# Performance work log

Measured on AMD Instinct MI355X. Metric: run time of the kernel, lower is better.

The kernel has to match this reference:

```python
import jax, jax.numpy as jnp
import numpy as np

B, S = 256, 512
E, K, D, H = 20000, 500, 128, 128  # num_exercises, num_skills, embed_dim, hidden_dim


def setup_inputs() -> dict:
    key = jax.random.key(0)
    ks = jax.random.split(key, 24)
    def lin(k, fan_in, fan_out):
        k1, k2 = jax.random.split(k)
        lim = 1.0 / np.sqrt(fan_in)
        W = jax.random.uniform(k1, (fan_in, fan_out), jnp.float32, -lim, lim)
        b = jax.random.uniform(k2, (fan_out,), jnp.float32, -lim, lim)
        return W, b
    def xavier(k, n, d):
        lim = np.sqrt(6.0 / (n + d))
        return jax.random.uniform(k, (n, d), jnp.float32, -lim, lim)
    W_time, b_time = lin(ks[0], 1, D)
    W_int, b_int = lin(ks[1], 4 * D, D)
    W_b1, b_b1 = lin(ks[2], 2, H)
    W_b2, b_b2 = lin(ks[3], H, H)
    W_learn, b_learn = lin(ks[4], H + D + 1 + H + H, H)
    W_forget, b_forget = lin(ks[5], H + D + H + H, H)
    W_pred, b_pred = lin(ks[6], H + D, 1)
    return {
        "exercise_seq": jax.random.randint(ks[7], (B, S), 0, E),
        "skill_seq": jax.random.randint(ks[8], (B, S), 0, K),
        "response_seq": jax.random.randint(ks[9], (B, S), 0, 2),
        "time_seq": jax.random.uniform(ks[10], (B, S), jnp.float32),
        "interval_seq": jax.random.uniform(ks[11], (B, S), jnp.float32),
        "attempt_seq": jax.random.uniform(ks[12], (B, S), jnp.float32),
        "hint_seq": jax.random.uniform(ks[13], (B, S), jnp.float32),
        "q_matrix": jax.random.uniform(ks[14], (E, K), jnp.float32),
        "exercise_emb": xavier(ks[15], E, D),
        "skill_emb": xavier(ks[16], K, D),
        "response_emb": xavier(ks[17], 2, D),
        "W_time": W_time, "b_time": b_time,
        "W_int": W_int, "b_int": b_int,
        "W_b1": W_b1, "b_b1": b_b1,
        "W_b2": W_b2, "b_b2": b_b2,
        "W_learn": W_learn, "b_learn": b_learn,
        "W_forget": W_forget, "b_forget": b_forget,
        "W_pred": W_pred, "b_pred": b_pred,
    }


def _forward(exercise_seq, skill_seq, response_seq, time_seq, interval_seq,
             attempt_seq, hint_seq, q_matrix,
             exercise_emb, skill_emb, response_emb,
             W_time, b_time, W_int, b_int, W_b1, b_b1, W_b2, b_b2,
             W_learn, b_learn, W_forget, b_forget, W_pred, b_pred):
    e = exercise_emb[exercise_seq]            # [B,S,D]
    s = skill_emb[skill_seq]                  # [B,S,D]
    r = response_emb[response_seq]            # [B,S,D]
    t = time_seq[..., None] * W_time[0] + b_time  # Linear(1,D): [B,S,D]
    inter = jax.nn.relu(jnp.concatenate([e, s, t, r], axis=-1) @ W_int + b_int)  # [B,S,D]
    beh_in = jnp.stack([attempt_seq, hint_seq], axis=-1)  # [B,S,2]
    beh = jax.nn.relu(beh_in @ W_b1 + b_b1) @ W_b2 + b_b2  # [B,S,H]
    # fifth gate input segment is behavior[:, t] except zeros at the last step
    beh2 = beh.at[:, -1, :].set(0.0)

    # time-major for scan
    xs = (jnp.swapaxes(e, 0, 1), jnp.swapaxes(inter, 0, 1),
          jnp.swapaxes(beh, 0, 1), jnp.swapaxes(beh2, 0, 1),
          jnp.swapaxes(interval_seq, 0, 1))
    h0 = jnp.zeros((e.shape[0], H), e.dtype)

    def step(h, x):
        ce, ci, cb, nb, iv = x
        lg = jax.nn.sigmoid(
            jnp.concatenate([h, ci, iv[:, None], cb, nb], axis=-1) @ W_learn + b_learn)
        fg = jax.nn.sigmoid(
            jnp.concatenate([h, ci, lg, cb], axis=-1) @ W_forget + b_forget)
        h = lg + fg * h
        p = jax.nn.sigmoid(jnp.concatenate([h, ce], axis=-1) @ W_pred + b_pred)
        return h, p[:, 0]

    _, preds = jax.lax.scan(step, h0, xs)  # [S,B]
    return jnp.swapaxes(preds, 0, 1)       # [B,S]


def reference(exercise_seq, skill_seq, response_seq, time_seq, interval_seq,
              attempt_seq, hint_seq, q_matrix,
              exercise_emb, skill_emb, response_emb,
              W_time, b_time, W_int, b_int, W_b1, b_b1, W_b2, b_b2,
              W_learn, b_learn, W_forget, b_forget, W_pred, b_pred):
    return _forward(exercise_seq, skill_seq, response_seq, time_seq, interval_seq,
                    attempt_seq, hint_seq, q_matrix,
                    exercise_emb, skill_emb, response_emb,
                    W_time, b_time, W_int, b_int, W_b1, b_b1, W_b2, b_b2,
                    W_learn, b_learn, W_forget, b_forget, W_pred, b_pred)
```

## Files before the change

### kernel.cpp

```cpp
#include <hip/hip_runtime.h>
#include <hip/hip_fp16.h>

#define BB 256
#define SS 512
#define EE_N 20000
#define NEGLAM -1.442695041f
typedef _Float16 f16;
typedef __attribute__((ext_vector_type(8))) _Float16 half8;
typedef __attribute__((ext_vector_type(4))) _Float16 half4_;
typedef __attribute__((ext_vector_type(2))) _Float16 half2_;
typedef __attribute__((ext_vector_type(4))) float f32x4;

__device__ __forceinline__ float sigm(float x) {
  return __builtin_amdgcn_rcpf(1.0f + __builtin_amdgcn_exp2f(NEGLAM * x));
}
__device__ __forceinline__ float sigm_pre(float s) {
  return __builtin_amdgcn_rcpf(1.0f + __builtin_amdgcn_exp2f(s));
}

__global__ __launch_bounds__(256) void k012_prep(
    const float* ex_emb, const float* skill_emb, const float* response_emb,
    const float* W_time, const float* b_time,
    const float* W_int, const float* b_int,
    const float* W_b2, const float* b_b2,
    const float* W_learn, const float* b_learn,
    const float* W_forget, const float* b_forget,
    const float* W_pred,
    float* Ee, float* Se, float* Re, float* Te, float* cbias,
    float* c_lg, float* c_fg, float* fix_l,
    float* M_lnb, f16* Wfrag, float* pe, f16* Bfrag) {
  __shared__ float es[8 * 128];
  int blk = blockIdx.x, tid = threadIdx.x;
  if (blk < 2500) {
    *(float4*)&es[tid * 4] = *(const float4*)&ex_emb[(size_t)blk * 1024 + tid * 4];
    __syncthreads();
    int d = tid & 127, rg = tid >> 7;
    float a0 = 0, a1 = 0, a2 = 0, a3 = 0;
    for (int k = 0; k < 128; k++) {
      float w = W_int[k * 128 + d];
      a0 += es[(rg * 4 + 0) * 128 + k] * w;
      a1 += es[(rg * 4 + 1) * 128 + k] * w;
      a2 += es[(rg * 4 + 2) * 128 + k] * w;
      a3 += es[(rg * 4 + 3) * 128 + k] * w;
    }
    Ee[((size_t)blk * 8 + rg * 4 + 0) * 128 + d] = a0;
    Ee[((size_t)blk * 8 + rg * 4 + 1) * 128 + d] = a1;
    Ee[((size_t)blk * 8 + rg * 4 + 2) * 128 + d] = a2;
    Ee[((size_t)blk * 8 + rg * 4 + 3) * 128 + d] = a3;
  } else if (blk < 3388) {
    int b0 = blk - 2500, j = tid;
    if (j < 128) {
      if (b0 < 500) {
        float a = 0.f;
        for (int k = 0; k < 128; k++) a += skill_emb[b0 * 128 + k] * W_int[(128 + k) * 128 + j];
        Se[b0 * 128 + j] = a;
      } else if (b0 < 502) {
        int i = b0 - 500; float a = 0.f;
        for (int k = 0; k < 128; k++) a += response_emb[i * 128 + k] * W_int[(384 + k) * 128 + j];
        Re[i * 128 + j] = a;
      } else if (b0 == 502) {
        float a = 0.f, c = 0.f;
        for (int k = 0; k < 128; k++) {
          float w = W_int[(256 + k) * 128 + j];
          a += W_time[k] * w; c += b_time[k] * w;
        }
        Te[j] = a; cbias[j] = b_int[j] + c;
      } else if (b0 < 503 + 128) {
        int k = b0 - 503;
        int kt = k >> 5, gg = (k >> 3) & 3, e = k & 7;
        int nct = j >> 4, cc = j & 15;
        float vL = NEGLAM * W_learn[(128 + k) * 128 + j];
        float vF = NEGLAM * W_forget[(128 + k) * 128 + j];
        Bfrag[((size_t)((nct * 8 + kt) * 64) + gg * 16 + cc) * 8 + e] = (f16)vL;
        Bfrag[((size_t)(((8 + nct) * 8 + kt) * 64) + gg * 16 + cc) * 8 + e] = (f16)vF;
      } else if (b0 < 631 + 128) {
        int k2 = b0 - 631; float a = 0.f, c = 0.f;
        for (int m = 0; m < 128; m++) {
          float w = W_b2[k2 * 128 + m];
          a += w * (W_learn[(257 + m) * 128 + j] + W_learn[(385 + m) * 128 + j]);
          c += w * W_forget[(384 + m) * 128 + j];
        }
        int krow = 128 + k2;
        int kt = krow >> 5, gg = (krow >> 3) & 3, e = krow & 7;
        int nct = j >> 4, cc = j & 15;
        Bfrag[((size_t)((nct * 8 + kt) * 64) + gg * 16 + cc) * 8 + e] = (f16)(NEGLAM * a);
        Bfrag[((size_t)(((8 + nct) * 8 + kt) * 64) + gg * 16 + cc) * 8 + e] = (f16)(NEGLAM * c);
      } else if (b0 < 759 + 128) {
        int k = b0 - 759; float a = 0.f;
        for (int m = 0; m < 128; m++) a += W_b2[k * 128 + m] * W_learn[(385 + m) * 128 + j];
        M_lnb[k * 128 + j] = NEGLAM * a;
      } else {
        float a = 0.f, c = 0.f, f = 0.f;
        for (int m = 0; m < 128; m++) {
          float w = b_b2[m];
          a += w * (W_learn[(257 + m) * 128 + j] + W_learn[(385 + m) * 128 + j]);
          c += w * W_forget[(384 + m) * 128 + j];
          f += w * W_learn[(385 + m) * 128 + j];
        }
        c_lg[j] = NEGLAM * (b_learn[j] + a);
        c_fg[j] = NEGLAM * (b_forget[j] + c);
        fix_l[j] = NEGLAM * f;
      }
    }
  } else if (blk < 3484) {
    int b2 = blk - 3388;
    if (tid < 64) {
      int mat = b2 >> 5, rem = b2 & 31, w = rem >> 2, t4 = rem & 3;
      int lane = tid, cc = lane & 15, gg = lane >> 4;
      const float* src = (mat == 0) ? W_learn : (mat == 1 ? W_forget : W_forget + 256 * 128);
      f16* dst = Wfrag + ((size_t)b2 * 64 + lane) * 8;
      #pragma unroll
      for (int e = 0; e < 8; e++) {
        int k = t4 * 32 + gg * 8 + e;
        int j = 16 * w + cc;
        dst[e] = (f16)(NEGLAM * src[k * 128 + j]);
      }
    }
  } else {
    int b3 = blk - 3484;
    int w = tid >> 6, l = tid & 63, g = l >> 4, li = l & 15;
    int row = b3 * 16 + w * 4 + g;
    const float4* ep = (const float4*)(ex_emb + (size_t)row * 128 + li * 8);
    const float4* wp = (const float4*)(W_pred + 128 + li * 8);
    float4 e0 = ep[0], e1 = ep[1], w0 = wp[0], w1 = wp[1];
    float s = e0.x * w0.x + e0.y * w0.y + e0.z * w0.z + e0.w * w0.w
            + e1.x * w1.x + e1.y * w1.y + e1.z * w1.z + e1.w * w1.w;
    #pragma unroll
    for (int m = 1; m < 16; m <<= 1) s += __shfl_xor(s, m);
    if (li == 0) pe[row] = s;
  }
}

__global__ __launch_bounds__(512) void k3_gemm_mfma(
    const int* ex_seq, const int* sk_seq, const int* re_seq,
    const float* time_seq, const float* interval_seq,
    const float* att_seq, const float* hint_seq,
    const float* W_b1, const float* b_b1,
    const float* Wiv,
    const float* Ee, const float* Se, const float* Re,
    const float* Te, const float* cbias,
    const float* c_lg, const float* c_fg,
    const f16* Bfrag, f16* PRE) {
  __shared__ _Float16 Ah[64 * 256];
  __shared__ float ivs[64];
  int tid = threadIdx.x;
  int w = tid >> 6, lane = tid & 63;
  int c = lane & 15, g = lane >> 4;
  int rowbase = blockIdx.x * 64;

  half8 bfr[2][8];
  const half8* bp = (const half8*)Bfrag;
  #pragma unroll
  for (int ncl = 0; ncl < 2; ncl++)
    #pragma unroll
    for (int kt = 0; kt < 8; kt++)
      bfr[ncl][kt] = bp[((size_t)((w * 2 + ncl) * 8 + kt)) * 64 + lane];

  {
    int r = tid & 63, seg = tid >> 6;
    int row = rowbase + r;
    if (seg == 0) ivs[r] = interval_seq[row];
    char* ab = (char*)Ah;
    if (seg < 4) {
      int ex = ex_seq[row], sk = sk_seq[row], rp = re_seq[row];
      float tm = time_seq[row];
      const float4* ee = (const float4*)(Ee + (size_t)ex * 128 + seg * 32);
      const float4* se = (const float4*)(Se + (size_t)sk * 128 + seg * 32);
      const float4* re = (const float4*)(Re + (size_t)rp * 128 + seg * 32);
      const float4* te = (const float4*)(Te + seg * 32);
      const float4* cb = (const float4*)(cbias + seg * 32);
      #pragma unroll
      for (int i8 = 0; i8 < 4; i8++) {
        half8 hv;
        #pragma unroll
        for (int q = 0; q < 2; q++) {
          float4 e4 = ee[i8 * 2 + q], s4 = se[i8 * 2 + q], r4 = re[i8 * 2 + q];
          float4 t4 = te[i8 * 2 + q], c4 = cb[i8 * 2 + q];
          hv[q * 4 + 0] = (_Float16)fmaxf(e4.x + s4.x + tm * t4.x + r4.x + c4.x, 0.f);
          hv[q * 4 + 1] = (_Float16)fmaxf(e4.y + s4.y + tm * t4.y + r4.y + c4.y, 0.f);
          hv[q * 4 + 2] = (_Float16)fmaxf(e4.z + s4.z + tm * t4.z + r4.z + c4.z, 0.f);
          hv[q * 4 + 3] = (_Float16)fmaxf(e4.w + s4.w + tm * t4.w + r4.w + c4.w, 0.f);
        }
        int k0 = seg * 32 + i8 * 8;
        int byte = r * 512 + k0 * 2; byte ^= ((r & 7) << 4);
        *(half8*)(ab + byte) = hv;
      }
    } else {
      int k2b_ = (seg - 4) * 32;
      float at = att_seq[row], hi = hint_seq[row];
      const float4* wa = (const float4*)(W_b1 + k2b_);
      const float4* wh = (const float4*)(W_b1 + 128 + k2b_);
      const float4* bb = (const float4*)(b_b1 + k2b_);
      #pragma unroll
      for (int i8 = 0; i8 < 4; i8++) {
        half8 hv;
        #pragma unroll
        for (int q = 0; q < 2; q++) {
          float4 a4 = wa[i8 * 2 + q], h4 = wh[i8 * 2 + q], b4 = bb[i8 * 2 + q];
          hv[q * 4 + 0] = (_Float16)fmaxf(at * a4.x + hi * h4.x + b4.x, 0.f);
          hv[q * 4 + 1] = (_Float16)fmaxf(at * a4.y + hi * h4.y + b4.y, 0.f);
          hv[q * 4 + 2] = (_Float16)fmaxf(at * a4.z + hi * h4.z + b4.z, 0.f);
          hv[q * 4 + 3] = (_Float16)fmaxf(at * a4.w + hi * h4.w + b4.w, 0.f);
        }
        int k0 = 128 + k2b_ + i8 * 8;
        int byte = r * 512 + k0 * 2; byte ^= ((r & 7) << 4);
        *(half8*)(ab + byte) = hv;
      }
    }
  }
  __syncthreads();

  f32x4 acc[4][2] = {};
  const char* ab = (const char*)Ah;
  #pragma unroll
  for (int kt = 0; kt < 8; kt++) {
    #pragma unroll
    for (int mr = 0; mr < 4; mr++) {
      int byte = (mr * 16 + c) * 512 + kt * 64 + g * 16; byte ^= ((c & 7) << 4);
      half8 a = *(const half8*)(ab + byte);
      acc[mr][0] = __builtin_amdgcn_mfma_f32_16x16x32_f16(a, bfr[0][kt], acc[mr][0], 0, 0, 0);
      acc[mr][1] = __builtin_amdgcn_mfma_f32_16x16x32_f16(a, bfr[1][kt], acc[mr][1], 0, 0, 0);
    }
  }

  bool isL = (w < 4);
  float addc[2], wiv[2];
  int coff[2];
  #pragma unroll
  for (int ncl = 0; ncl < 2; ncl++) {
    int j = w * 32 + ncl * 16 + c;
    if (isL) { addc[ncl] = c_lg[j]; wiv[ncl] = NEGLAM * Wiv[j]; coff[ncl] = j * 4; }
    else     { addc[ncl] = c_fg[j - 128]; wiv[ncl] = 0.f; coff[ncl] = (j - 128) * 4 + 1; }
  }
  #pragma unroll
  for (int mr = 0; mr < 4; mr++) {
    #pragma unroll
    for (int rr = 0; rr < 4; rr++) {
      int rl = mr * 16 + g * 4 + rr;
      int row = rowbase + rl;
      float iv = ivs[rl];
      size_t base = (size_t)(row >> 9) * 131072 + (size_t)((row & 511) >> 1) * 512 + (row & 1) * 2;
      #pragma unroll
      for (int ncl = 0; ncl < 2; ncl++) {
        float v = acc[mr][ncl][rr] + addc[ncl] + iv * wiv[ncl];
        PRE[base + coff[ncl]] = (f16)v;
      }
    }
  }
}

__global__ __launch_bounds__(128) void k4_fix(
    const float* att_seq, const float* hint_seq,
    const float* W_b1, const float* b_b1,
    const float* M_lnb, const float* fix_l, f16* PRE) {
  int b = blockIdx.x, j = threadIdx.x;
  int row = b * SS + (SS - 1);
  __shared__ float rb_s[128];
  float v = att_seq[row] * W_b1[j] + hint_seq[row] * W_b1[128 + j] + b_b1[j];
  rb_s[j] = fmaxf(v, 0.f);
  __syncthreads();
  float a = fix_l[j];
  for (int m = 0; m < 128; m++) a += rb_s[m] * M_lnb[m * 128 + j];
  size_t idx = (size_t)b * 131072 + 255 * 512 + 2 + j * 4;
  PRE[idx] = (f16)((float)PRE[idx] - a);
}

#define BAR() asm volatile("s_waitcnt lgkmcnt(0)\n\ts_barrier" ::: "memory")
#define MF(A, B, C) __builtin_amdgcn_mfma_f32_16x16x32_f16(A, B, C, 0, 0, 0)

__global__ __launch_bounds__(512, 2) void k5_scan_mfma(
    const f16* __restrict__ PRE, const f16* __restrict__ Wfrag,
    f16* __restrict__ h_blk) {
  __shared__ _Float16 AhA[2048], AhB[2048], Alg[2048];
  int tid = threadIdx.x;
  int w = tid >> 6, lane = tid & 63;
  int c = lane & 15, g = lane >> 4;
  int b = blockIdx.x;

  if (tid < 256) {
    ((float4*)AhA)[tid] = make_float4(0.f, 0.f, 0.f, 0.f);
    ((float4*)AhB)[tid] = make_float4(0.f, 0.f, 0.f, 0.f);
    ((float4*)Alg)[tid] = make_float4(0.f, 0.f, 0.f, 0.f);
  }

  half8 bL[4], bFH[4], bFL[4];
  const half8* wp = (const half8*)Wfrag;
  #pragma unroll
  for (int t4 = 0; t4 < 4; t4++) {
    bL [t4] = wp[((0 * 8 + w) * 4 + t4) * 64 + lane];
    bFH[t4] = wp[((1 * 8 + w) * 4 + t4) * 64 + lane];
    bFL[t4] = wp[((2 * 8 + w) * 4 + t4) * 64 + lane];
  }

  int rd[4], wr[2];
  #pragma unroll
  for (int t4 = 0; t4 < 4; t4++) {
    int K8 = 4 * t4 + g;
    rd[t4] = K8 * 256 + (c ^ (K8 & 3)) * 16;
  }
  {
    int F = 16 * w + c;
    int K8w = F >> 3, q = K8w & 3;
    #pragma unroll
    for (int r = 0; r < 2; r++)
      wr[r] = K8w * 256 + ((4 * g + r) ^ q) * 16 + (F & 7) * 2;
  }

  int col = 16 * w + c;
  const f16* pr[2]; f16* hb4[2];
  float hstate[2] = {0.f, 0.f};
  float lgf[2];
  half4_ pA[4][2], pB[4][2];
  half4_ hb[2];
  #pragma unroll
  for (int r = 0; r < 2; r++) {
    int br = b * 8 + g * 2 + r;
    pr[r]  = PRE + (size_t)br * 131072 + col * 4;
    hb4[r] = h_blk + (size_t)br * 65536 + col * 4;
  }
  #pragma unroll
  for (int p = 0; p < 4; p++)
    #pragma unroll
    for (int r = 0; r < 2; r++)
      pA[p][r] = *(const half4_*)((const char*)pr[r] + p * 1024);
  __syncthreads();

  const f32x4 Z4 = {0.f, 0.f, 0.f, 0.f};

#define STEPX(SRC, DST, CB, P, PAR, LB, LOFF, I0, TIN, FLUSH, DOINC)             \
  {                                                                              \
    half8 ha[4];                                                                 \
    _Pragma("unroll")                                                            \
    for (int t4 = 0; t4 < 4; t4++)                                               \
      ha[t4] = *(const half8*)((const char*)(SRC) + rd[t4]);                     \
    if (DOINC) {                                                                 \
      _Pragma("unroll")                                                          \
      for (int r = 0; r < 2; r++) pr[r] += 4096;                                 \
    }                                                                            \
    { const int p_ = (I0) >> 1, r_ = (I0) & 1;                                   \
      LB[p_][r_] = *(const half4_*)((const char*)pr[r_] + (LOFF) + p_ * 1024); } \
    f32x4 cL = Z4, cF = Z4;                                                      \
    _Pragma("unroll")                                                            \
    for (int r = 0; r < 2; r++) {                                                \
      cL[r] = (float)CB[P][r][(PAR) * 2];                                        \
      cF[r] = (float)CB[P][r][(PAR) * 2 + 1];                                    \
    }                                                                            \
    __builtin_amdgcn_s_setprio(1);                                               \
    f32x4 aLa = cL, aLb = Z4;                                                    \
    aLa = MF(ha[0], bL[0], aLa);                                                 \
    aLb = MF(ha[2], bL[2], aLb);                                                 \
    aLa = MF(ha[1], bL[1], aLa);                                                 \
    aLb = MF(ha[3], bL[3], aLb);                                                 \
    __builtin_amdgcn_s_setprio(0);                                               \
    _Pragma("unroll")                                                            \
    for (int r = 0; r < 2; r++) {                                                \
      lgf[r] = sigm_pre(aLa[r] + aLb[r]);                                        \
      *(_Float16*)((char*)Alg + wr[r]) = (_Float16)lgf[r];                       \
    }                                                                            \
    BAR();                                                                       \
    half8 la[4];                                                                 \
    _Pragma("unroll")                                                            \
    for (int t4 = 0; t4 < 4; t4++)                                               \
      la[t4] = *(const half8*)((const char*)Alg + rd[t4]);                       \
    __builtin_amdgcn_s_setprio(1);                                               \
    f32x4 aHa = cF, aHb = Z4;                                                    \
    aHa = MF(ha[0], bFH[0], aHa);                                                \
    aHb = MF(ha[2], bFH[2], aHb);                                                \
    aHa = MF(ha[1], bFH[1], aHa);                                                \
    aHb = MF(ha[3], bFH[3], aHb);                                                \
    aHa = MF(la[0], bFL[0], aHa);                                                \
    aHb = MF(la[2], bFL[2], aHb);                                                \
    aHa = MF(la[1], bFL[1], aHa);                                                \
    aHb = MF(la[3], bFL[3], aHb);                                                \
    __builtin_amdgcn_s_setprio(0);                                               \
    _Pragma("unroll")                                                            \
    for (int r = 0; r < 2; r++) {                                                \
      float fg = sigm_pre(aHa[r] + aHb[r]);                                      \
      float hn = lgf[r] + fg * hstate[r];                                        \
      hstate[r] = hn;                                                            \
      _Float16 hv = (_Float16)hn;                                                \
      *(_Float16*)((char*)(DST) + wr[r]) = hv;                                   \
      hb[r][TIN] = hv;                                                           \
    }                                                                            \
    if ((FLUSH) >= 0) {                                                          \
      _Pragma("unroll")                                                          \
      for (int r = 0; r < 2; r++)                                                \
        *(half4_*)((char*)hb4[r] + (FLUSH)) = hb[r];                             \
    }                                                                            \
    BAR();                                                                       \
  }

  for (int it = 0; it < 32; ++it) {
    STEPX(AhA, AhB, pA, 0, 0, pB, 4096, 0, 0,   -1, 0);
    STEPX(AhB, AhA, pA, 0, 1, pB, 4096, 1, 1,   -1, 0);
    STEPX(AhA, AhB, pA, 1, 0, pB, 4096, 2, 2,   -1, 0);
    STEPX(AhB, AhA, pA, 1, 1, pB, 4096, 3, 3,    0, 0);
    STEPX(AhA, AhB, pA, 2, 0, pB, 4096, 4, 0,   -1, 0);
    STEPX(AhB, AhA, pA, 2, 1, pB, 4096, 5, 1,   -1, 0);
    STEPX(AhA, AhB, pA, 3, 0, pB, 4096, 6, 2,   -1, 0);
    STEPX(AhB, AhA, pA, 3, 1, pB, 4096, 7, 3, 1024, 0);
    STEPX(AhA, AhB, pB, 0, 0, pA, 0,    0, 0,   -1, 1);
    STEPX(AhB, AhA, pB, 0, 1, pA, 0,    1, 1,   -1, 0);
    STEPX(AhA, AhB, pB, 1, 0, pA, 0,    2, 2,   -1, 0);
    STEPX(AhB, AhA, pB, 1, 1, pA, 0,    3, 3, 2048, 0);
    STEPX(AhA, AhB, pB, 2, 0, pA, 0,    4, 0,   -1, 0);
    STEPX(AhB, AhA, pB, 2, 1, pA, 0,    5, 1,   -1, 0);
    STEPX(AhA, AhB, pB, 3, 0, pA, 0,    6, 2,   -1, 0);
    STEPX(AhB, AhA, pB, 3, 1, pA, 0,    7, 3, 3072, 0);
    #pragma unroll
    for (int r = 0; r < 2; r++) hb4[r] += 2048;
  }
#undef STEPX
}

__global__ __launch_bounds__(256) void k6_pred(
    const f16* h_blk, const int* ex_seq, const float* pe,
    const float* W_pred, const float* b_pred, float* out) {
  int tid = threadIdx.x;
  int wv = tid >> 6, lane = tid & 63;
  int task = blockIdx.x * 4 + wv;
  int br = task >> 7, t4b = task & 127;
  const f16* hp = h_blk + ((size_t)br * 128 + t4b) * 128 * 4;
  half4_ h0 = *(const half4_*)(hp + lane * 4);
  half4_ h1 = *(const half4_*)(hp + (lane + 64) * 4);
  float w0 = W_pred[lane], w1 = W_pred[lane + 64];
  float s[4];
  #pragma unroll
  for (int q = 0; q < 4; q++) s[q] = (float)h0[q] * w0 + (float)h1[q] * w1;
  #pragma unroll
  for (int m = 1; m < 64; m <<= 1) {
    #pragma unroll
    for (int q = 0; q < 4; q++) s[q] += __shfl_xor(s[q], m);
  }
  if (lane == 0) {
    int4 ex = *(const int4*)(ex_seq + (size_t)br * 512 + t4b * 4);
    float bb = b_pred[0];
    float4 o;
    o.x = sigm(s[0] + pe[ex.x] + bb);
    o.y = sigm(s[1] + pe[ex.y] + bb);
    o.z = sigm(s[2] + pe[ex.z] + bb);
    o.w = sigm(s[3] + pe[ex.w] + bb);
    *(float4*)(out + (size_t)br * 512 + t4b * 4) = o;
  }
}

extern "C" void kernel_launch(void* const* d_in, const int* in_sizes, int n_in,
                              void* d_out, int out_size, void* d_ws, size_t ws_size,
                              hipStream_t stream) {
  const int*   ex_seq   = (const int*)d_in[0];
  const int*   sk_seq   = (const int*)d_in[1];
  const int*   re_seq   = (const int*)d_in[2];
  const float* time_seq = (const float*)d_in[3];
  const float* interval_seq = (const float*)d_in[4];
  const float* att_seq  = (const float*)d_in[5];
  const float* hint_seq = (const float*)d_in[6];
  const float* ex_emb   = (const float*)d_in[8];
  const float* sk_emb   = (const float*)d_in[9];
  const float* re_emb   = (const float*)d_in[10];
  const float* W_time   = (const float*)d_in[11];
  const float* b_time   = (const float*)d_in[12];
  const float* W_int    = (const float*)d_in[13];
  const float* b_int    = (const float*)d_in[14];
  const float* W_b1     = (const float*)d_in[15];
  const float* b_b1     = (const float*)d_in[16];
  const float* W_b2     = (const float*)d_in[17];
  const float* b_b2     = (const float*)d_in[18];
  const float* W_learn  = (const float*)d_in[19];
  const float* b_learn  = (const float*)d_in[20];
  const float* W_forget = (const float*)d_in[21];
  const float* b_forget = (const float*)d_in[22];
  const float* W_pred   = (const float*)d_in[23];
  const float* b_pred   = (const float*)d_in[24];

  char* ws = (char*)d_ws;
  float* Ee    = (float*)(ws);
  float* Se    = (float*)(ws + 10240000);
  float* Re    = (float*)(ws + 10496000);
  float* Te    = (float*)(ws + 10497024);
  float* cbias = (float*)(ws + 10497536);
  float* c_lg  = (float*)(ws + 10498048);
  float* c_fg  = (float*)(ws + 10498560);
  float* fix_l = (float*)(ws + 10499072);
  float* M_lnb = (float*)(ws + 10761728);
  f16*   PRE   = (f16*)  (ws + 10827264);
  f16*   h_blk = (f16*)  (ws + 77936128);
  f16*   Wfrag = (f16*)  (ws + 111490560);
  float* pe    = (float*)(ws + 111588864);
  f16*   Bfrag = (f16*)  (ws + 77936128);

  k012_prep<<<dim3(4734), dim3(256), 0, stream>>>(
      ex_emb, sk_emb, re_emb, W_time, b_time, W_int, b_int, W_b2, b_b2,
      W_learn, b_learn, W_forget, b_forget, W_pred,
      Ee, Se, Re, Te, cbias, c_lg, c_fg, fix_l, M_lnb, Wfrag, pe, Bfrag);
  k3_gemm_mfma<<<dim3(2048), dim3(512), 0, stream>>>(
      ex_seq, sk_seq, re_seq, time_seq, interval_seq, att_seq, hint_seq,
      W_b1, b_b1, W_learn + 256 * 128, Ee, Se, Re, Te, cbias, c_lg, c_fg, Bfrag, PRE);
  k4_fix<<<dim3(256), dim3(128), 0, stream>>>(
      att_seq, hint_seq, W_b1, b_b1, M_lnb, fix_l, PRE);
  k5_scan_mfma<<<dim3(32), dim3(512), 0, stream>>>(PRE, Wfrag, h_blk);
  k6_pred<<<dim3(8192), dim3(256), 0, stream>>>(
      h_blk, ex_seq, pe, W_pred, b_pred, (float*)d_out);
}
```

Measured before the change: 328.3 us.

## Halve batch rows per scan block and double scan grid

The recurrent scan kernel now gives each block 4 batch rows instead of 8: each lane tracks one row rather than two, and the launch grid grows from 32 to 64 blocks. The serial per-step chain stays the same length, but more CUs run at once and each thread has less per-step epilogue work. In exchange, MFMA tiles are only a quarter populated (one valid row per 4-row group), and total weight fragment loads and LDS traffic double across blocks.

```diff
diff --git a/kernel.cpp b/kernel.cpp
--- a/kernel.cpp
+++ b/kernel.cpp
@@ -292,7 +292,7 @@
     bFL[t4] = wp[((2 * 8 + w) * 4 + t4) * 64 + lane];
   }
 
-  int rd[4], wr[2];
+  int rd[4], wr0;
   #pragma unroll
   for (int t4 = 0; t4 < 4; t4++) {
     int K8 = 4 * t4 + g;
@@ -301,28 +301,20 @@
   {
     int F = 16 * w + c;
     int K8w = F >> 3, q = K8w & 3;
-    #pragma unroll
-    for (int r = 0; r < 2; r++)
-      wr[r] = K8w * 256 + ((4 * g + r) ^ q) * 16 + (F & 7) * 2;
+    wr0 = K8w * 256 + ((4 * g) ^ q) * 16 + (F & 7) * 2;
   }
 
   int col = 16 * w + c;
-  const f16* pr[2]; f16* hb4[2];
-  float hstate[2] = {0.f, 0.f};
-  float lgf[2];
-  half4_ pA[4][2], pB[4][2];
-  half4_ hb[2];
-  #pragma unroll
-  for (int r = 0; r < 2; r++) {
-    int br = b * 8 + g * 2 + r;
-    pr[r]  = PRE + (size_t)br * 131072 + col * 4;
-    hb4[r] = h_blk + (size_t)br * 65536 + col * 4;
-  }
+  int br = b * 4 + g;
+  const f16* pr0 = PRE + (size_t)br * 131072 + col * 4;
+  f16* hb40 = h_blk + (size_t)br * 65536 + col * 4;
+  float hstate = 0.f;
+  float lgf0;
+  half4_ pA[4], pB[4];
+  half4_ hb0;
   #pragma unroll
   for (int p = 0; p < 4; p++)
-    #pragma unroll
-    for (int r = 0; r < 2; r++)
-      pA[p][r] = *(const half4_*)((const char*)pr[r] + p * 1024);
+    pA[p] = *(const half4_*)((const char*)pr0 + p * 1024);
   __syncthreads();
 
   const f32x4 Z4 = {0.f, 0.f, 0.f, 0.f};
@@ -333,18 +325,12 @@
     _Pragma("unroll")                                                            \
     for (int t4 = 0; t4 < 4; t4++)                                               \
       ha[t4] = *(const half8*)((const char*)(SRC) + rd[t4]);                     \
-    if (DOINC) {                                                                 \
-      _Pragma("unroll")                                                          \
-      for (int r = 0; r < 2; r++) pr[r] += 4096;                                 \
-    }                                                                            \
-    { const int p_ = (I0) >> 1, r_ = (I0) & 1;                                   \
-      LB[p_][r_] = *(const half4_*)((const char*)pr[r_] + (LOFF) + p_ * 1024); } \
+    if (DOINC) pr0 += 4096;                                                      \
+    if ((I0) >= 0)                                                               \
+      LB[(I0)] = *(const half4_*)((const char*)pr0 + (LOFF) + (I0) * 1024);      \
     f32x4 cL = Z4, cF = Z4;                                                      \
-    _Pragma("unroll")                                                            \
-    for (int r = 0; r < 2; r++) {                                                \
-      cL[r] = (float)CB[P][r][(PAR) * 2];                                        \
-      cF[r] = (float)CB[P][r][(PAR) * 2 + 1];                                    \
-    }                                                                            \
+    cL[0] = (float)CB[P][(PAR) * 2];                                             \
+    cF[0] = (float)CB[P][(PAR) * 2 + 1];                                         \
     __builtin_amdgcn_s_setprio(1);                                               \
     f32x4 aLa = cL, aLb = Z4;                                                    \
     aLa = MF(ha[0], bL[0], aLa);                                                 \
@@ -352,11 +338,8 @@
     aLa = MF(ha[1], bL[1], aLa);                                                 \
     aLb = MF(ha[3], bL[3], aLb);                                                 \
     __builtin_amdgcn_s_setprio(0);                                               \
-    _Pragma("unroll")                                                            \
-    for (int r = 0; r < 2; r++) {                                                \
-      lgf[r] = sigm_pre(aLa[r] + aLb[r]);                                        \
-      *(_Float16*)((char*)Alg + wr[r]) = (_Float16)lgf[r];                       \
-    }                                                                            \
+    lgf0 = sigm_pre(aLa[0] + aLb[0]);                                            \
+    *(_Float16*)((char*)Alg + wr0) = (_Float16)lgf0;                             \
     BAR();                                                                       \
     half8 la[4];                                                                 \
     _Pragma("unroll")                                                            \
@@ -373,42 +356,37 @@
     aHa = MF(la[1], bFL[1], aHa);                                                \
     aHb = MF(la[3], bFL[3], aHb);                                                \
     __builtin_amdgcn_s_setprio(0);                                               \
-    _Pragma("unroll")                                                            \
-    for (int r = 0; r < 2; r++) {                                                \
-      float fg = sigm_pre(aHa[r] + aHb[r]);                                      \
-      float hn = lgf[r] + fg * hstate[r];                                        \
-      hstate[r] = hn;                                                            \
+    {                                                                            \
+      float fg = sigm_pre(aHa[0] + aHb[0]);                                      \
+      float hn = lgf0 + fg * hstate;                                             \
+      hstate = hn;                                                               \
       _Float16 hv = (_Float16)hn;                                                \
-      *(_Float16*)((char*)(DST) + wr[r]) = hv;                                   \
-      hb[r][TIN] = hv;                                                           \
+      *(_Float16*)((char*)(DST) + wr0) = hv;                                     \
+      hb0[TIN] = hv;                                                             \
     }                                                                            \
-    if ((FLUSH) >= 0) {                                                          \
-      _Pragma("unroll")                                                          \
-      for (int r = 0; r < 2; r++)                                                \
-        *(half4_*)((char*)hb4[r] + (FLUSH)) = hb[r];                             \
-    }                                                                            \
+    if ((FLUSH) >= 0)                                                            \
+      *(half4_*)((char*)hb40 + (FLUSH)) = hb0;                                   \
     BAR();                                                                       \
   }
 
   for (int it = 0; it < 32; ++it) {
-    STEPX(AhA, AhB, pA, 0, 0, pB, 4096, 0, 0,   -1, 0);
-    STEPX(AhB, AhA, pA, 0, 1, pB, 4096, 1, 1,   -1, 0);
-    STEPX(AhA, AhB, pA, 1, 0, pB, 4096, 2, 2,   -1, 0);
-    STEPX(AhB, AhA, pA, 1, 1, pB, 4096, 3, 3,    0, 0);
-    STEPX(AhA, AhB, pA, 2, 0, pB, 4096, 4, 0,   -1, 0);
-    STEPX(AhB, AhA, pA, 2, 1, pB, 4096, 5, 1,   -1, 0);
-    STEPX(AhA, AhB, pA, 3, 0, pB, 4096, 6, 2,   -1, 0);
-    STEPX(AhB, AhA, pA, 3, 1, pB, 4096, 7, 3, 1024, 0);
-    STEPX(AhA, AhB, pB, 0, 0, pA, 0,    0, 0,   -1, 1);
-    STEPX(AhB, AhA, pB, 0, 1, pA, 0,    1, 1,   -1, 0);
-    STEPX(AhA, AhB, pB, 1, 0, pA, 0,    2, 2,   -1, 0);
-    STEPX(AhB, AhA, pB, 1, 1, pA, 0,    3, 3, 2048, 0);
-    STEPX(AhA, AhB, pB, 2, 0, pA, 0,    4, 0,   -1, 0);
-    STEPX(AhB, AhA, pB, 2, 1, pA, 0,    5, 1,   -1, 0);
-    STEPX(AhA, AhB, pB, 3, 0, pA, 0,    6, 2,   -1, 0);
-    STEPX(AhB, AhA, pB, 3, 1, pA, 0,    7, 3, 3072, 0);
-    #pragma unroll
-    for (int r = 0; r < 2; r++) hb4[r] += 2048;
+    STEPX(AhA, AhB, pA, 0, 0, pB, 4096,  0, 0,   -1, 0);
+    STEPX(AhB, AhA, pA, 0, 1, pB, 4096, -1, 1,   -1, 0);
+    STEPX(AhA, AhB, pA, 1, 0, pB, 4096,  1, 2,   -1, 0);
+    STEPX(AhB, AhA, pA, 1, 1, pB, 4096, -1, 3,    0, 0);
+    STEPX(AhA, AhB, pA, 2, 0, pB, 4096,  2, 0,   -1, 0);
+    STEPX(AhB, AhA, pA, 2, 1, pB, 4096, -1, 1,   -1, 0);
+    STEPX(AhA, AhB, pA, 3, 0, pB, 4096,  3, 2,   -1, 0);
+    STEPX(AhB, AhA, pA, 3, 1, pB, 4096, -1, 3, 1024, 0);
+    STEPX(AhA, AhB, pB, 0, 0, pA, 0,     0, 0,   -1, 1);
+    STEPX(AhB, AhA, pB, 0, 1, pA, 0,    -1, 1,   -1, 0);
+    STEPX(AhA, AhB, pB, 1, 0, pA, 0,     1, 2,   -1, 0);
+    STEPX(AhB, AhA, pB, 1, 1, pA, 0,    -1, 3, 2048, 0);
+    STEPX(AhA, AhB, pB, 2, 0, pA, 0,     2, 0,   -1, 0);
+    STEPX(AhB, AhA, pB, 2, 1, pA, 0,    -1, 1,   -1, 0);
+    STEPX(AhA, AhB, pB, 3, 0, pA, 0,     3, 2,   -1, 0);
+    STEPX(AhB, AhA, pB, 3, 1, pA, 0,    -1, 3, 3072, 0);
+    hb40 += 2048;
   }
 #undef STEPX
 }
@@ -497,7 +475,7 @@
       W_b1, b_b1, W_learn + 256 * 128, Ee, Se, Re, Te, cbias, c_lg, c_fg, Bfrag, PRE);
   k4_fix<<<dim3(256), dim3(128), 0, stream>>>(
       att_seq, hint_seq, W_b1, b_b1, M_lnb, fix_l, PRE);
-  k5_scan_mfma<<<dim3(32), dim3(512), 0, stream>>>(PRE, Wfrag, h_blk);
+  k5_scan_mfma<<<dim3(64), dim3(512), 0, stream>>>(PRE, Wfrag, h_blk);
   k6_pred<<<dim3(8192), dim3(256), 0, stream>>>(
       h_blk, ex_seq, pe, W_pred, b_pred, (float*)d_out);
 }
```

Measured after the change: 300.3 us. -8.5%, faster.
